# Kernel optimization log

Hardware: AMD Instinct MI355X
Metric: run time of the kernel (lower is better)

## Reference

```python
import jax, jax.numpy as jnp
import numpy as np

B, S, D_MODEL, D_HEAD = 8, 2048, 1024, 128
MAX_ROUNDS = 3
THRESH = 0.1
SCALE = 1.0 / np.sqrt(float(D_HEAD))


def setup_inputs() -> dict:
    key = jax.random.key(0)
    ks = jax.random.split(key, 12)

    def lin(k, out_d, in_d):
        # torch Linear weight layout [out, in], y = x @ W.T + b
        return (jax.random.normal(k, (out_d, in_d), jnp.float32) / np.sqrt(float(in_d))).astype(jnp.float32)

    thesis_w = lin(ks[3], D_HEAD, D_HEAD)
    return {
        "x": jax.random.normal(ks[0], (B, S, D_MODEL), jnp.float32),
        "wq": lin(ks[1], D_HEAD, D_MODEL),
        "wk": lin(ks[2], D_HEAD, D_MODEL),
        "wv": lin(ks[4], D_HEAD, D_MODEL),
        "thesis_w": thesis_w,  # antithesis weight is -thesis_w per __init__
        "thesis_b": 0.02 * jax.random.normal(ks[5], (D_HEAD,), jnp.float32),
        "anti_b": 0.02 * jax.random.normal(ks[6], (D_HEAD,), jnp.float32),
        "s_w1": lin(ks[7], D_HEAD, 3 * D_HEAD),
        "s_b1": jnp.zeros((D_HEAD,), jnp.float32),
        "s_w2": lin(ks[8], D_HEAD, D_HEAD),
        "s_b2": jnp.zeros((D_HEAD,), jnp.float32),
        "g_w": lin(ks[9], 1, 2 * D_HEAD),
        "g_b": jnp.zeros((1,), jnp.float32),
    }


def reference(x, wq, wk, wv, thesis_w, thesis_b, anti_b, s_w1, s_b1, s_w2, s_b2, g_w, g_b):
    # q/k/v projections (no bias)
    q = jnp.einsum("bsm,hm->bsh", x, wq)
    k = jnp.einsum("bsm,hm->bsh", x, wk)
    v = jnp.einsum("bsm,hm->bsh", x, wv)

    attn = jax.nn.softmax(jnp.einsum("bqh,bkh->bqk", q, k) * SCALE, axis=-1)
    # dropout is identity at eval time
    cur = jnp.einsum("bqk,bkh->bqh", attn, v)  # [B,S,Dh]

    # attn_weights and v never change across rounds, so thesis/antithesis are
    # round-invariant: compute the context projections once.
    context = cur
    thesis = context @ thesis_w.T + thesis_b
    anti = context @ (-thesis_w).T + anti_b  # antithesis weight = -thesis weight

    active = jnp.ones((B, S), dtype=bool)
    for _ in range(MAX_ROUNDS):
        # emulate `if not active_mask.any(): break` under jit
        any_active = jnp.any(active)
        am = active[..., None].astype(x.dtype)
        at, aa, ac = thesis * am, anti * am, cur * am

        h = jax.nn.relu(jnp.concatenate([at, aa, ac], axis=-1) @ s_w1.T + s_b1)
        synth = h @ s_w2.T + s_b2
        gate = jax.nn.sigmoid(jnp.concatenate([ac, synth], axis=-1) @ g_w.T + g_b)
        update = gate * (synth - ac) * 0.1
        new = cur + update  # applied to ALL tokens, matching original

        stable = jnp.linalg.norm(update, axis=-1) < THRESH  # new - cur == update
        cur = jnp.where(any_active, new, cur)
        active = jnp.where(any_active, active & ~stable, active)
    return cur
```

## Files before the change

### kernel.cpp

```cpp
#include <hip/hip_runtime.h>
#include <hip/hip_bf16.h>

#define B_   8
#define S_   2048
#define DM   1024
#define DH   128
#define BS_  16384
#define SCALE_  0.08838834764831845f
#define SCALE2_ 0.12751744f

typedef unsigned short u16;
typedef unsigned int   u32;
typedef _Float16 half8 __attribute__((ext_vector_type(8)));
typedef __bf16   bf16x8 __attribute__((ext_vector_type(8)));
typedef float    f32x4 __attribute__((ext_vector_type(4)));
typedef u32      u32x4 __attribute__((ext_vector_type(4)));

union H8 { u32x4 v; u32 u[4]; half8 h; bf16x8 b; };

__device__ __forceinline__ float bf2f(u16 u) {
    union { u32 i; float f; } w; w.i = ((u32)u) << 16; return w.f;
}
__device__ __forceinline__ void unpack8(uint4 v, float* f) {
    f[0] = bf2f(v.x & 0xffff); f[1] = bf2f(v.x >> 16);
    f[2] = bf2f(v.y & 0xffff); f[3] = bf2f(v.y >> 16);
    f[4] = bf2f(v.z & 0xffff); f[5] = bf2f(v.z >> 16);
    f[6] = bf2f(v.w & 0xffff); f[7] = bf2f(v.w >> 16);
}
__device__ __forceinline__ float ldE(const void* b, size_t i, int isbf16) {
    return isbf16 ? bf2f(((const u16*)b)[i]) : ((const float*)b)[i];
}
__device__ __forceinline__ void ld8(const void* b, size_t i, int isbf16, float* f) {
    if (isbf16) {
        unpack8(*(const uint4*)((const u16*)b + i), f);
    } else {
        float4 a = *(const float4*)((const float*)b + i);
        float4 c = *(const float4*)((const float*)b + i + 4);
        f[0] = a.x; f[1] = a.y; f[2] = a.z; f[3] = a.w;
        f[4] = c.x; f[5] = c.y; f[6] = c.z; f[7] = c.w;
    }
}
__device__ __forceinline__ u32 f2pk(float v) {
    _Float16 h = (_Float16)v;
    _Float16 l = (_Float16)(v - (float)h);
    union { _Float16 f; u16 u; } a, b; a.f = h; b.f = l;
    return ((u32)a.u << 16) | (u32)b.u;
}
__device__ __forceinline__ void split8(const float* f, u32x4& hi, u32x4& lo) {
    u32 H[8], L[8];
#pragma unroll
    for (int j = 0; j < 8; ++j) {
        _Float16 h = (_Float16)f[j];
        _Float16 l = (_Float16)(f[j] - (float)h);
        union { _Float16 x; u16 u; } a, b; a.x = h; b.x = l;
        H[j] = a.u; L[j] = b.u;
    }
    hi = (u32x4){H[0] | (H[1] << 16), H[2] | (H[3] << 16), H[4] | (H[5] << 16), H[6] | (H[7] << 16)};
    lo = (u32x4){L[0] | (L[1] << 16), L[2] | (L[3] << 16), L[4] | (L[5] << 16), L[6] | (L[7] << 16)};
}
__device__ __forceinline__ u32 permHI(u32 eB, u32 eA) { return __builtin_amdgcn_perm(eB, eA, 0x07060302u); }
__device__ __forceinline__ u16 f2h(float v) { union { _Float16 f; u16 u; } a; a.f = (_Float16)v; return a.u; }
__device__ __forceinline__ float h2f(u16 u) { union { _Float16 f; u16 u; } a; a.u = u; return (float)a.f; }

__global__ void init_kernel(const void* x, int* flag, int* active, int* counts) {
    int i = blockIdx.x * 256 + threadIdx.x;
    if (i < BS_) active[i] = 1;
    if (i < 4) counts[i] = (i == 0) ? BS_ : 0;
    if (i == 0) {
        const u16* w = (const u16*)x;
        int sane = 0;
        for (int t = 0; t < 256; ++t) {
            int e = (w[2 * t] >> 7) & 0xFF;
            if (e >= 100 && e <= 135) ++sane;
        }
        *flag = (sane >= 192) ? 1 : 0;
    }
}

__global__ __launch_bounds__(256) void prepack_w_kernel(
    const void* __restrict__ wq, const void* __restrict__ wk, const void* __restrict__ wv,
    const int* __restrict__ flag, u32x4* __restrict__ wpk)
{
    const int isb = *flag;
    const int gid = blockIdx.x * 256 + threadIdx.x;
    const int l  = gid & 63;
    const int t  = (gid >> 6) & 7;
    const int ks = (gid >> 9) & 31;
    const int z  = gid >> 14;
    const void* W = (z == 0) ? wq : (z == 1) ? wk : wv;
    const int row = 16 * t + (l & 15);
    const int k0  = ks * 32 + 8 * (l >> 4);
    const size_t base = ((((size_t)z * 32 + ks) * 16) + 2 * t) * 64 + l;
    if (isb) {
        uint4 v = *(const uint4*)((const u16*)W + (size_t)row * DM + k0);
        wpk[base] = (u32x4){v.x, v.y, v.z, v.w};
    } else {
        float f[8];
        ld8(W, (size_t)row * DM + k0, 0, f);
        u32x4 hi, lo;
        split8(f, hi, lo);
        wpk[base]      = hi;
        wpk[base + 64] = lo;
    }
}

__global__ __launch_bounds__(256) void qkv_kernel(
    const void* __restrict__ x, const u32x4* __restrict__ wpk,
    const int* __restrict__ flag, u32* __restrict__ qout,
    u32x4* __restrict__ kfrag, u32x4* __restrict__ vfrag)
{
    const int isb = *flag;
    const int z = blockIdx.z;
    const int bx = blockIdx.x;
    const int m0 = ((bx & 7) * 32 + (bx >> 3)) * 64;
    const int tid = threadIdx.x;
    const int wave = tid >> 6, lane = tid & 63;
    const int qd = lane >> 4, c = lane & 15;

    __shared__ u32x4 WL[2][8][2][64];
    __shared__ u16 TS[64][136];

    const u32x4* wz = wpk + (size_t)z * (32 * 16 * 64);
    const size_t arow = (size_t)(m0 + wave * 16 + c) * DM + 8 * qd;

#define STAGE_W(ks_, b_)                                                          \
    {                                                                             \
        const u32x4* _src = wz + ((size_t)(ks_) * 16 + 4 * wave) * 64 + lane;     \
        _Pragma("unroll")                                                         \
        for (int _j = 0; _j < 4; ++_j) {                                          \
            __builtin_amdgcn_global_load_lds(                                     \
                (const __attribute__((address_space(1))) u32*)(_src + _j * 64),   \
                (__attribute__((address_space(3))) u32*)&WL[b_][2 * wave + (_j >> 1)][_j & 1][0], \
                16, 0, 0);                                                        \
        }                                                                         \
    }
#define STAGE_WH(ks_, b_)                                                         \
    {                                                                             \
        _Pragma("unroll")                                                         \
        for (int _j = 0; _j < 2; ++_j) {                                          \
            __builtin_amdgcn_global_load_lds(                                     \
                (const __attribute__((address_space(1))) u32*)(                   \
                    wz + ((size_t)(ks_) * 16 + 2 * (2 * wave + _j)) * 64 + lane), \
                (__attribute__((address_space(3))) u32*)&WL[b_][2 * wave + _j][0][0], \
                16, 0, 0);                                                        \
        }                                                                         \
    }

    f32x4 acc[8] = {};

    if (isb) {
        const u16* xb = (const u16*)x;
        uint4 Ab = *(const uint4*)(xb + arow);
        STAGE_WH(0, 0);
        uint4 Abn = *(const uint4*)(xb + arow + 32);
        __syncthreads();
        for (int ks = 0; ks < 32; ++ks) {
            const int cb = ks & 1;
            if (ks + 1 < 32) STAGE_WH(ks + 1, cb ^ 1);
            H8 Ah; Ah.v = (u32x4){Ab.x, Ab.y, Ab.z, Ab.w};
#pragma unroll
            for (int t = 0; t < 8; ++t) {
                H8 bh; bh.v = WL[cb][t][0][lane];
                acc[t] = __builtin_amdgcn_mfma_f32_16x16x32_bf16(Ah.b, bh.b, acc[t], 0, 0, 0);
            }
            Ab = Abn;
            if (ks + 2 < 32) Abn = *(const uint4*)(xb + arow + (size_t)(ks + 2) * 32);
            __syncthreads();
        }
    } else {
        float Ar[8], Arn[8];
        ld8(x, arow, 0, Ar);
        STAGE_W(0, 0);
        ld8(x, arow + 32, 0, Arn);
        __syncthreads();
        for (int ks = 0; ks < 32; ++ks) {
            const int cb = ks & 1;
            if (ks + 1 < 32) STAGE_W(ks + 1, cb ^ 1);
            H8 Ah, Al;
            split8(Ar, Ah.v, Al.v);
#pragma unroll
            for (int t = 0; t < 8; ++t) {
                H8 bh, bl;
                bh.v = WL[cb][t][0][lane]; bl.v = WL[cb][t][1][lane];
                acc[t] = __builtin_amdgcn_mfma_f32_16x16x32_f16(Al.h, bh.h, acc[t], 0, 0, 0);
                acc[t] = __builtin_amdgcn_mfma_f32_16x16x32_f16(Ah.h, bl.h, acc[t], 0, 0, 0);
                acc[t] = __builtin_amdgcn_mfma_f32_16x16x32_f16(Ah.h, bh.h, acc[t], 0, 0, 0);
            }
#pragma unroll
            for (int j = 0; j < 8; ++j) Ar[j] = Arn[j];
            if (ks + 2 < 32) ld8(x, arow + (size_t)(ks + 2) * 32, 0, Arn);
            __syncthreads();
        }
    }
#undef STAGE_W
#undef STAGE_WH

    if (z == 0) {
#pragma unroll
        for (int r = 0; r < 4; ++r) {
            const int row = m0 + wave * 16 + qd * 4 + r;
            u32* op = qout + (size_t)row * DH + c;
#pragma unroll
            for (int t = 0; t < 8; ++t) op[t * 16] = f2pk(acc[t][r]);
        }
    } else {
#pragma unroll
        for (int t = 0; t < 8; ++t)
#pragma unroll
            for (int r = 0; r < 4; ++r)
                TS[wave * 16 + qd * 4 + r][16 * t + c] = f2h(acc[t][r]);
        __syncthreads();
        if (z == 1) {
#pragma unroll
            for (int i = 0; i < 4; ++i) {
                const int f = tid + 256 * i;
                const int lf = f & 63, ks = (f >> 6) & 3, sub = f >> 8;
                const int key = sub * 16 + (lf & 15);
                const int d0  = ks * 32 + 8 * (lf >> 4);
                u32 w[4];
#pragma unroll
                for (int q = 0; q < 4; ++q)
                    w[q] = (u32)TS[key][d0 + 2 * q] | ((u32)TS[key][d0 + 2 * q + 1] << 16);
                kfrag[((size_t)(m0 / 16 + sub) * 4 + ks) * 64 + lf] = (u32x4){w[0], w[1], w[2], w[3]};
            }
        } else {
#pragma unroll
            for (int i = 0; i < 4; ++i) {
                const int f = tid + 256 * i;
                const int lf = f & 63, t = (f >> 6) & 7, sub = f >> 9;
                const int kb2 = sub * 32 + 8 * (lf >> 4);
                const int dh  = 16 * t + (lf & 15);
                u32 w[4];
#pragma unroll
                for (int q = 0; q < 4; ++q)
                    w[q] = (u32)TS[kb2 + 2 * q][dh] | ((u32)TS[kb2 + 2 * q + 1][dh] << 16);
                vfrag[((size_t)(m0 / 32 + sub) * 8 + t) * 64 + lf] = (u32x4){w[0], w[1], w[2], w[3]};
            }
        }
    }
}

template <bool WRITE_PARTIAL>
__device__ __forceinline__ void attn_body(
    const u32* qp, const u32x4* __restrict__ kfrag, const u32x4* __restrict__ vfrag,
    u16* outO, u16* outL, float* cur,
    int b, int q0, int kt0, int kt1, int part)
{
    const int tid = threadIdx.x;
    const int wave = tid >> 6, lane = tid & 63;
    const int qd = lane >> 4, c = lane & 15;

    __shared__ u16 PB[4][531];

    H8 Qh[4];
    {
        const u32* qr = qp + ((size_t)b * S_ + q0 + wave * 16 + c) * DH;
#pragma unroll
        for (int ks = 0; ks < 4; ++ks) {
            uint4 e0 = *(const uint4*)(qr + ks * 32 + qd * 8);
            uint4 e1 = *(const uint4*)(qr + ks * 32 + qd * 8 + 4);
            Qh[ks].u[0] = permHI(e0.y, e0.x); Qh[ks].u[1] = permHI(e0.w, e0.z);
            Qh[ks].u[2] = permHI(e1.y, e1.x); Qh[ks].u[3] = permHI(e1.w, e1.z);
        }
    }

    f32x4 O[8] = {};
    float lsum[4] = {};

    const u32x4* kb0 = kfrag + (size_t)b * 128 * 256;
    const u32x4* vb0 = vfrag + (size_t)b * 64 * 512;

    for (int kt = kt0; kt < kt1; ++kt) {
        const u32x4* kf = kb0 + (size_t)kt * 512;
        const u32x4* vf = vb0 + (size_t)kt * 512;

        f32x4 S0 = {}, S1 = {};
#pragma unroll
        for (int ks = 0; ks < 4; ++ks) {
            H8 kh;
            kh.v = kf[ks * 64 + lane];
            S0 = __builtin_amdgcn_mfma_f32_16x16x32_f16(Qh[ks].h, kh.h, S0, 0, 0, 0);
            kh.v = kf[256 + ks * 64 + lane];
            S1 = __builtin_amdgcn_mfma_f32_16x16x32_f16(Qh[ks].h, kh.h, S1, 0, 0, 0);
        }

        u16* pw = PB[wave];
#pragma unroll
        for (int r = 0; r < 4; ++r) {
            float e0 = exp2f(fmaf(S0[r], SCALE2_, -4.0f));
            float e1 = exp2f(fmaf(S1[r], SCALE2_, -4.0f));
            lsum[r] += e0 + e1;
            pw[(4 * qd + r) * 33 + c]      = f2h(e0);
            pw[(4 * qd + r) * 33 + 16 + c] = f2h(e1);
        }

        u16 e[8];
#pragma unroll
        for (int j = 0; j < 8; ++j) e[j] = pw[c * 33 + 8 * qd + j];
        H8 Ph;
        Ph.u[0] = (u32)e[0] | ((u32)e[1] << 16);
        Ph.u[1] = (u32)e[2] | ((u32)e[3] << 16);
        Ph.u[2] = (u32)e[4] | ((u32)e[5] << 16);
        Ph.u[3] = (u32)e[6] | ((u32)e[7] << 16);

#pragma unroll
        for (int t = 0; t < 8; ++t) {
            H8 vh;
            vh.v = vf[t * 64 + lane];
            O[t] = __builtin_amdgcn_mfma_f32_16x16x32_f16(Ph.h, vh.h, O[t], 0, 0, 0);
        }
    }

    if (WRITE_PARTIAL) {
        float lred[4];
#pragma unroll
        for (int r = 0; r < 4; ++r) {
            float l = lsum[r];
            l += __shfl_xor(l, 1); l += __shfl_xor(l, 2);
            l += __shfl_xor(l, 4); l += __shfl_xor(l, 8);
            lred[r] = l;
        }
        const size_t rb = (size_t)b * S_ + q0 + wave * 16 + 4 * qd;
        u16* Op = outO + (size_t)part * ((size_t)BS_ * DH);
#pragma unroll
        for (int t = 0; t < 8; ++t)
#pragma unroll
            for (int r = 0; r < 4; ++r)
                Op[(rb + r) * DH + t * 16 + c] = f2h(O[t][r]);
        if (c == 0) {
            u16* lp = outL + (size_t)part * BS_;
#pragma unroll
            for (int r = 0; r < 4; ++r) lp[rb + r] = f2h(lred[r]);
        }
    } else {
        float linv[4];
#pragma unroll
        for (int r = 0; r < 4; ++r) {
            float l = lsum[r];
            l += __shfl_xor(l, 1); l += __shfl_xor(l, 2);
            l += __shfl_xor(l, 4); l += __shfl_xor(l, 8);
            linv[r] = 1.0f / l;
        }
        const size_t rb = (size_t)b * S_ + q0 + wave * 16 + 4 * qd;
#pragma unroll
        for (int t = 0; t < 8; ++t)
#pragma unroll
            for (int r = 0; r < 4; ++r)
                cur[(rb + r) * DH + t * 16 + c] = O[t][r] * linv[r];
    }
}

__global__ __launch_bounds__(256) void attn_kernel(
    const u32* qp, const u32x4* __restrict__ kfrag, const u32x4* __restrict__ vfrag, float* cur)
{
    const int rid = blockIdx.x + 32 * blockIdx.y;
    attn_body<false>(qp, kfrag, vfrag, nullptr, nullptr, cur,
                     rid & 7, ((rid >> 3) & 31) * 64, 0, S_ / 32, 0);
}

__global__ __launch_bounds__(256) void attn_split_kernel(
    const u32* qp, const u32x4* __restrict__ kfrag, const u32x4* __restrict__ vfrag,
    u16* __restrict__ Opart, u16* __restrict__ lpart)
{
    const int rid = blockIdx.x + 32 * (blockIdx.y + 8 * blockIdx.z);
    const int b    = rid & 7;
    const int qx   = (rid >> 3) & 31;
    const int part = rid >> 8;
    const int quart = S_ / 128;
    attn_body<true>(qp, kfrag, vfrag, Opart, lpart, nullptr,
                    b, qx * 64, part * quart, (part + 1) * quart, part);
}

__global__ __launch_bounds__(256) void combine_kernel(
    const u16* __restrict__ Opart, const u16* __restrict__ lpart,
    float* __restrict__ cur)
{
    const size_t N1 = (size_t)BS_ * DH;
    const size_t i0 = ((size_t)blockIdx.x * 256 + threadIdx.x) * 16;
    const int row = (int)(i0 >> 7);
    const float lt = h2f(lpart[row]) + h2f(lpart[BS_ + row])
                   + h2f(lpart[2 * BS_ + row]) + h2f(lpart[3 * BS_ + row]);
    const float linv = 1.0f / lt;
    float acc[16] = {};
#pragma unroll
    for (int p = 0; p < 4; ++p) {
        const u16* op = Opart + (size_t)p * N1 + i0;
        uint4 v0 = *(const uint4*)op;
        uint4 v1 = *(const uint4*)(op + 8);
        const u32 w[8] = {v0.x, v0.y, v0.z, v0.w, v1.x, v1.y, v1.z, v1.w};
#pragma unroll
        for (int j = 0; j < 8; ++j) {
            acc[2 * j]     += h2f((u16)(w[j] & 0xffff));
            acc[2 * j + 1] += h2f((u16)(w[j] >> 16));
        }
    }
#pragma unroll
    for (int t = 0; t < 4; ++t)
        *(float4*)(cur + i0 + t * 4) = make_float4(
            acc[4*t] * linv, acc[4*t+1] * linv, acc[4*t+2] * linv, acc[4*t+3] * linv);
}

__global__ __launch_bounds__(256) void prepack_rw_kernel(
    const void* __restrict__ tw, const void* __restrict__ w1, const void* __restrict__ w2,
    const int* __restrict__ flag, u32x4* __restrict__ pk)
{
    const int isb = *flag;
    const int gid = blockIdx.x * 256 + threadIdx.x;
    const int l = gid & 63, t = (gid >> 6) & 7, ks = (gid >> 9) & 3, mat = gid >> 11;
    const int row = 16 * t + (l & 15);
    const int k0  = ks * 32 + 8 * (l >> 4);
    float f[8];
    if (mat == 0)      ld8(tw, (size_t)row * DH + k0, isb, f);
    else if (mat <= 3) ld8(w1, (size_t)row * 384 + (mat - 1) * 128 + k0, isb, f);
    else               ld8(w2, (size_t)row * DH + k0, isb, f);
    u32x4 hi, lo;
    split8(f, hi, lo);
    const size_t base = (((size_t)mat * 4 + ks) * 16 + 2 * t) * 64 + l;
    pk[base] = hi; pk[base + 64] = lo;
}

struct Afrag { H8 h[4], l[4]; };
__device__ __forceinline__ void splitA(const float (&A)[4][8], Afrag& F) {
#pragma unroll
    for (int ks = 0; ks < 4; ++ks) split8(A[ks], F.h[ks].v, F.l[ks].v);
}
__device__ __forceinline__ void gemm_wb(const Afrag& F, const u32x4 (*WB)[16][64],
                                        const int lane, const int isb, f32x4 (&acc)[8])
{
#pragma unroll
    for (int ks = 0; ks < 4; ++ks) {
#pragma unroll
        for (int t = 0; t < 8; ++t) {
            H8 bh, bl;
            bh.v = WB[ks][2 * t][lane];
            bl.v = WB[ks][2 * t + 1][lane];
            acc[t] = __builtin_amdgcn_mfma_f32_16x16x32_f16(F.l[ks].h, bh.h, acc[t], 0, 0, 0);
            if (!isb)
                acc[t] = __builtin_amdgcn_mfma_f32_16x16x32_f16(F.h[ks].h, bl.h, acc[t], 0, 0, 0);
            acc[t] = __builtin_amdgcn_mfma_f32_16x16x32_f16(F.h[ks].h, bh.h, acc[t], 0, 0, 0);
        }
    }
}

__global__ __launch_bounds__(256) void round_kernel(
    const float* cur0, const float* curr,
    const u32x4* __restrict__ pk,
    const void* __restrict__ tb, const void* __restrict__ ab,
    const void* __restrict__ b1, const void* __restrict__ b2,
    const void* __restrict__ gw, const void* __restrict__ gb,
    const int* __restrict__ flag, int* active, int* counts, int r,
    float* cur_out, void* dout)
{
    const int isb = *flag;
    const int tok0 = blockIdx.x * 64;
    const int tid = threadIdx.x;
    const bool last = (dout != nullptr);

    if (counts[r] <= 0) {
        if (last) {
            for (int e = tid; e < 64 * DH; e += 256) {
                size_t idx = (size_t)tok0 * DH + e;
                float v = curr[idx];
                if (isb) ((__hip_bfloat16*)dout)[idx] = __float2bfloat16(v);
                else     ((float*)dout)[idx] = v;
            }
        }
        return;
    }

    const int wave = tid >> 6, lane = tid & 63;
    const int qd = lane >> 4, c = lane & 15;

    __shared__ u32x4 WB[4][16][64];
    __shared__ float T0S[64][132];
    __shared__ float HSS[64][132];
    __shared__ float actS[64], tbS[128], abS[128], b1S[128], b2S[128], gwS[256];
    __shared__ int blkcnt;

#define STAGE_RW(mat_)                                                             \
    {                                                                              \
        _Pragma("unroll")                                                          \
        for (int _j = 0; _j < 16; ++_j) {                                          \
            __builtin_amdgcn_global_load_lds(                                      \
                (const __attribute__((address_space(1))) u32*)(                    \
                    pk + (((size_t)(mat_) * 4 + wave) * 16 + _j) * 64 + lane),     \
                (__attribute__((address_space(3))) u32*)&WB[wave][_j][0],          \
                16, 0, 0);                                                         \
        }                                                                          \
    }

    STAGE_RW(0);
    if (tid < 64) actS[tid] = active[tok0 + tid] ? 1.0f : 0.0f;
    if (tid < 128) {
        tbS[tid] = ldE(tb, tid, isb); abS[tid] = ldE(ab, tid, isb);
        b1S[tid] = ldE(b1, tid, isb); b2S[tid] = ldE(b2, tid, isb);
    }
    gwS[tid] = ldE(gw, tid, isb);
    if (tid == 0) blkcnt = 0;
    const float gbf = ldE(gb, 0, isb);

    const int rowl = 16 * wave + c;
    const int hr   = 16 * wave + 4 * qd;

    float A1[4][8];
    {
        const float* cr = cur0 + (size_t)(tok0 + rowl) * DH;
#pragma unroll
        for (int ks = 0; ks < 4; ++ks) {
            *(float4*)&A1[ks][0] = *(const float4*)(cr + ks * 32 + 8 * qd);
            *(float4*)&A1[ks][4] = *(const float4*)(cr + ks * 32 + 8 * qd + 4);
        }
    }
    Afrag FA; splitA(A1, FA);
    __syncthreads();

    {
        f32x4 acc[8] = {};
        gemm_wb(FA, WB, lane, isb, acc);
#pragma unroll
        for (int t = 0; t < 8; ++t)
#pragma unroll
            for (int rr = 0; rr < 4; ++rr)
                T0S[hr + rr][16 * t + c] = acc[t][rr];
    }
    __syncthreads();
    STAGE_RW(1);

    f32x4 acc1[8] = {};
    const float am_r = actS[rowl];
    {
        float Ac[4][8];
#pragma unroll
        for (int ks = 0; ks < 4; ++ks)
#pragma unroll
            for (int j = 0; j < 8; ++j) {
                const int k = ks * 32 + 8 * qd + j;
                Ac[ks][j] = (T0S[rowl][k] + tbS[k]) * am_r;
            }
        Afrag FC; splitA(Ac, FC);
        __syncthreads();
        gemm_wb(FC, WB, lane, isb, acc1);
    }
    __syncthreads();
    STAGE_RW(2);
    {
        float Ac[4][8];
#pragma unroll
        for (int ks = 0; ks < 4; ++ks)
#pragma unroll
            for (int j = 0; j < 8; ++j) {
                const int k = ks * 32 + 8 * qd + j;
                Ac[ks][j] = (abS[k] - T0S[rowl][k]) * am_r;
            }
        Afrag FC; splitA(Ac, FC);
        __syncthreads();
        gemm_wb(FC, WB, lane, isb, acc1);
    }
    __syncthreads();
    STAGE_RW(3);
    {
        float Ac[4][8];
        const float* cr = curr + (size_t)(tok0 + rowl) * DH;
#pragma unroll
        for (int ks = 0; ks < 4; ++ks) {
            float4 a0 = *(const float4*)(cr + ks * 32 + 8 * qd);
            float4 a1 = *(const float4*)(cr + ks * 32 + 8 * qd + 4);
            Ac[ks][0] = a0.x * am_r; Ac[ks][1] = a0.y * am_r;
            Ac[ks][2] = a0.z * am_r; Ac[ks][3] = a0.w * am_r;
            Ac[ks][4] = a1.x * am_r; Ac[ks][5] = a1.y * am_r;
            Ac[ks][6] = a1.z * am_r; Ac[ks][7] = a1.w * am_r;
        }
        Afrag FC; splitA(Ac, FC);
        __syncthreads();
        gemm_wb(FC, WB, lane, isb, acc1);
    }
#pragma unroll
    for (int t = 0; t < 8; ++t)
#pragma unroll
        for (int rr = 0; rr < 4; ++rr)
            HSS[hr + rr][16 * t + c] = fmaxf(acc1[t][rr] + b1S[16 * t + c], 0.0f);
    __syncthreads();
    STAGE_RW(4);
    {
        float Ac[4][8];
#pragma unroll
        for (int ks = 0; ks < 4; ++ks) {
            const float* hp = &HSS[rowl][ks * 32 + 8 * qd];
            *(float4*)&Ac[ks][0] = *(const float4*)hp;
            *(float4*)&Ac[ks][4] = *(const float4*)(hp + 4);
        }
        Afrag FC; splitA(Ac, FC);
        __syncthreads();
        f32x4 acc2[8] = {};
        gemm_wb(FC, WB, lane, isb, acc2);
#pragma unroll
        for (int t = 0; t < 8; ++t)
#pragma unroll
            for (int rr = 0; rr < 4; ++rr)
                T0S[hr + rr][16 * t + c] = acc2[t][rr] + b2S[16 * t + c];
    }
    __syncthreads();

    const int tok = tid >> 2, d0 = (tid & 3) * 32;
    const float am = actS[tok];
    const float* cp = curr + (size_t)(tok0 + tok) * DH + d0;
    float cv[32];
#pragma unroll
    for (int t = 0; t < 8; ++t) {
        float4 vv = *(const float4*)(cp + t * 4);
        cv[t * 4] = vv.x; cv[t * 4 + 1] = vv.y; cv[t * 4 + 2] = vv.z; cv[t * 4 + 3] = vv.w;
    }
    const float* srow = &T0S[tok][d0];
    float gp = 0.0f;
#pragma unroll
    for (int e = 0; e < 32; ++e)
        gp += cv[e] * am * gwS[d0 + e] + srow[e] * gwS[128 + d0 + e];
    gp += __shfl_xor(gp, 1, 4);
    gp += __shfl_xor(gp, 2, 4);
    const float gate = 1.0f / (1.0f + __expf(-(gp + gbf)));
    float ss = 0.0f; float up[32];
#pragma unroll
    for (int e = 0; e < 32; ++e) {
        float u = gate * (srow[e] - cv[e] * am) * 0.1f;
        up[e] = u; ss += u * u;
    }
    ss += __shfl_xor(ss, 1, 4);
    ss += __shfl_xor(ss, 2, 4);
    const bool stable = sqrtf(ss) < 0.1f;

    if (last) {
        size_t off = (size_t)(tok0 + tok) * DH + d0;
        if (isb) {
            __hip_bfloat16* op = (__hip_bfloat16*)dout + off;
#pragma unroll
            for (int e = 0; e < 32; ++e) op[e] = __float2bfloat16(cv[e] + up[e]);
        } else {
            float* op = (float*)dout + off;
#pragma unroll
            for (int t = 0; t < 8; ++t)
                *(float4*)(op + t * 4) = make_float4(cv[t * 4] + up[t * 4], cv[t * 4 + 1] + up[t * 4 + 1],
                                                     cv[t * 4 + 2] + up[t * 4 + 2], cv[t * 4 + 3] + up[t * 4 + 3]);
        }
    } else {
        float* op = cur_out + (size_t)(tok0 + tok) * DH + d0;
#pragma unroll
        for (int t = 0; t < 8; ++t)
            *(float4*)(op + t * 4) = make_float4(cv[t * 4] + up[t * 4], cv[t * 4 + 1] + up[t * 4 + 1],
                                                 cv[t * 4 + 2] + up[t * 4 + 2], cv[t * 4 + 3] + up[t * 4 + 3]);
    }
    const int newact = (am > 0.0f && !stable) ? 1 : 0;
    if ((tid & 3) == 0) {
        active[tok0 + tok] = newact;
        if (newact) atomicAdd(&blkcnt, 1);
    }
    __syncthreads();
    if (tid == 0 && blkcnt > 0) atomicAdd(&counts[r + 1], blkcnt);
#undef STAGE_RW
}

extern "C" void kernel_launch(void* const* d_in, const int* in_sizes, int n_in,
                              void* d_out, int out_size, void* d_ws, size_t ws_size,
                              hipStream_t stream) {
    const void* x  = d_in[0];
    const void* wq = d_in[1];
    const void* wk = d_in[2];
    const void* wv = d_in[3];
    const void* tw = d_in[4];
    const void* tb = d_in[5];
    const void* ab = d_in[6];
    const void* w1 = d_in[7];
    const void* b1 = d_in[8];
    const void* w2 = d_in[9];
    const void* b2 = d_in[10];
    const void* gw = d_in[11];
    const void* gb = d_in[12];

    u32* ws = (u32*)d_ws;
    const size_t N1 = (size_t)BS_ * DH;
    u32* qp = ws;
    u32* kp = ws + N1;
    u32* vp = ws + 2 * N1;
    int* active = (int*)(ws + 3 * N1);
    int* counts = active + BS_;
    int* flag   = counts + 4;
    float* cur0  = (float*)qp;
    float* cur_r = (float*)kp;
    u16* Opart16 = (u16*)(ws + 3 * N1 + 32768);
    u16* lpart16 = (u16*)(ws + 5 * N1 + 32768);
    const bool big_ws = ws_size >= (size_t)42300000;
    u32x4* wpk = (u32x4*)(ws + 3 * N1 + 32768);
    u32x4* pkRW = (u32x4*)vp;
    u32x4* kfragP = (u32x4*)kp;
    u32x4* vfragP = (u32x4*)vp;

    init_kernel<<<dim3(BS_ / 256), 256, 0, stream>>>(x, flag, active, counts);
    prepack_w_kernel<<<dim3(192), 256, 0, stream>>>(wq, wk, wv, flag, wpk);
    qkv_kernel<<<dim3(BS_ / 64, 1, 3), 256, 0, stream>>>(x, wpk, flag, qp, kfragP, vfragP);
    if (big_ws) {
        attn_split_kernel<<<dim3(S_ / 64, B_, 4), 256, 0, stream>>>(qp, kfragP, vfragP, Opart16, lpart16);
        combine_kernel<<<dim3(512), 256, 0, stream>>>(Opart16, lpart16, cur0);
    } else {
        attn_kernel<<<dim3(S_ / 64, B_), 256, 0, stream>>>(qp, kfragP, vfragP, cur0);
    }
    prepack_rw_kernel<<<dim3(40), 256, 0, stream>>>(tw, w1, w2, flag, pkRW);
    round_kernel<<<dim3(BS_ / 64), 256, 0, stream>>>(
        cur0, cur0, pkRW, tb, ab, b1, b2, gw, gb, flag, active, counts, 0, cur_r, nullptr);
    round_kernel<<<dim3(BS_ / 64), 256, 0, stream>>>(
        cur0, cur_r, pkRW, tb, ab, b1, b2, gw, gb, flag, active, counts, 1, cur_r, nullptr);
    round_kernel<<<dim3(BS_ / 64), 256, 0, stream>>>(
        cur0, cur_r, pkRW, tb, ab, b1, b2, gw, gb, flag, active, counts, 2, cur_r, d_out);
}
```

Baseline: 266.5 us.

## Shrink LDS footprint in qkv and round kernels to raise occupancy

In qkv_kernel, the weight buffer and the transpose scratch now share one aliased LDS array, and the bf16 path stages two k-slices per barrier, halving the number of syncs. In round_kernel, the weight staging buffer is halved: the bf16 path loads only hi parts, and the fp32 path stages in two halves with extra barriers. The intermediate T0S/HSS tiles are stored as fp16 instead of fp32. The aim is to cut LDS use so more blocks fit per CU. The cost is extra barriers in the fp32 path and fp16 rounding of intermediates, which may change accuracy.

```diff
diff --git a/kernel.cpp b/kernel.cpp
--- a/kernel.cpp
+++ b/kernel.cpp
@@ -117,12 +117,26 @@
     const int wave = tid >> 6, lane = tid & 63;
     const int qd = lane >> 4, c = lane & 15;
 
-    __shared__ u32x4 WL[2][8][2][64];
-    __shared__ u16 TS[64][136];
+    __shared__ u32x4 WLraw[2][16][64];
+    u32x4 (*WLb)[2][8][64] = (u32x4(*)[2][8][64])WLraw;
+    u32x4 (*WLf)[8][2][64] = (u32x4(*)[8][2][64])WLraw;
+    u16 (*TS)[136] = (u16(*)[136])WLraw;
 
     const u32x4* wz = wpk + (size_t)z * (32 * 16 * 64);
     const size_t arow = (size_t)(m0 + wave * 16 + c) * DM + 8 * qd;
 
+#define STAGE2(i_, b_)                                                            \
+    {                                                                             \
+        _Pragma("unroll")                                                         \
+        for (int _j = 0; _j < 4; ++_j) {                                          \
+            const int _g = wave * 4 + _j, _ksub = _g >> 3, _t = _g & 7;           \
+            __builtin_amdgcn_global_load_lds(                                     \
+                (const __attribute__((address_space(1))) u32*)(                   \
+                    wz + ((size_t)(2 * (i_) + _ksub) * 16 + 2 * _t) * 64 + lane), \
+                (__attribute__((address_space(3))) u32*)&WLb[b_][_ksub][_t][0],   \
+                16, 0, 0);                                                        \
+        }                                                                         \
+    }
 #define STAGE_W(ks_, b_)                                                          \
     {                                                                             \
         const u32x4* _src = wz + ((size_t)(ks_) * 16 + 4 * wave) * 64 + lane;     \
@@ -130,41 +144,41 @@
         for (int _j = 0; _j < 4; ++_j) {                                          \
             __builtin_amdgcn_global_load_lds(                                     \
                 (const __attribute__((address_space(1))) u32*)(_src + _j * 64),   \
-                (__attribute__((address_space(3))) u32*)&WL[b_][2 * wave + (_j >> 1)][_j & 1][0], \
+                (__attribute__((address_space(3))) u32*)&WLf[b_][2 * wave + (_j >> 1)][_j & 1][0], \
                 16, 0, 0);                                                        \
         }                                                                         \
     }
-#define STAGE_WH(ks_, b_)                                                         \
-    {                                                                             \
-        _Pragma("unroll")                                                         \
-        for (int _j = 0; _j < 2; ++_j) {                                          \
-            __builtin_amdgcn_global_load_lds(                                     \
-                (const __attribute__((address_space(1))) u32*)(                   \
-                    wz + ((size_t)(ks_) * 16 + 2 * (2 * wave + _j)) * 64 + lane), \
-                (__attribute__((address_space(3))) u32*)&WL[b_][2 * wave + _j][0][0], \
-                16, 0, 0);                                                        \
-        }                                                                         \
-    }
 
     f32x4 acc[8] = {};
 
     if (isb) {
         const u16* xb = (const u16*)x;
-        uint4 Ab = *(const uint4*)(xb + arow);
-        STAGE_WH(0, 0);
-        uint4 Abn = *(const uint4*)(xb + arow + 32);
+        uint4 A0 = *(const uint4*)(xb + arow);
+        uint4 A1 = *(const uint4*)(xb + arow + 32);
+        STAGE2(0, 0);
+        uint4 A0n = *(const uint4*)(xb + arow + 64);
+        uint4 A1n = *(const uint4*)(xb + arow + 96);
         __syncthreads();
-        for (int ks = 0; ks < 32; ++ks) {
-            const int cb = ks & 1;
-            if (ks + 1 < 32) STAGE_WH(ks + 1, cb ^ 1);
-            H8 Ah; Ah.v = (u32x4){Ab.x, Ab.y, Ab.z, Ab.w};
+        for (int i = 0; i < 16; ++i) {
+            const int cb = i & 1;
+            if (i + 1 < 16) STAGE2(i + 1, cb ^ 1);
+            H8 Ah0; Ah0.v = (u32x4){A0.x, A0.y, A0.z, A0.w};
+            H8 Ah1; Ah1.v = (u32x4){A1.x, A1.y, A1.z, A1.w};
 #pragma unroll
             for (int t = 0; t < 8; ++t) {
-                H8 bh; bh.v = WL[cb][t][0][lane];
-                acc[t] = __builtin_amdgcn_mfma_f32_16x16x32_bf16(Ah.b, bh.b, acc[t], 0, 0, 0);
-            }
-            Ab = Abn;
-            if (ks + 2 < 32) Abn = *(const uint4*)(xb + arow + (size_t)(ks + 2) * 32);
+                H8 bh; bh.v = WLb[cb][0][t][lane];
+                acc[t] = __builtin_amdgcn_mfma_f32_16x16x32_bf16(Ah0.b, bh.b, acc[t], 0, 0, 0);
+            }
+#pragma unroll
+            for (int t = 0; t < 8; ++t) {
+                H8 bh; bh.v = WLb[cb][1][t][lane];
+                acc[t] = __builtin_amdgcn_mfma_f32_16x16x32_bf16(Ah1.b, bh.b, acc[t], 0, 0, 0);
+            }
+            A0 = A0n; A1 = A1n;
+            if (i + 2 < 16) {
+                A0n = *(const uint4*)(xb + arow + (size_t)(i + 2) * 64);
+                A1n = *(const uint4*)(xb + arow + (size_t)(i + 2) * 64 + 32);
+            }
             __syncthreads();
         }
     } else {
@@ -181,7 +195,7 @@
 #pragma unroll
             for (int t = 0; t < 8; ++t) {
                 H8 bh, bl;
-                bh.v = WL[cb][t][0][lane]; bl.v = WL[cb][t][1][lane];
+                bh.v = WLf[cb][t][0][lane]; bl.v = WLf[cb][t][1][lane];
                 acc[t] = __builtin_amdgcn_mfma_f32_16x16x32_f16(Al.h, bh.h, acc[t], 0, 0, 0);
                 acc[t] = __builtin_amdgcn_mfma_f32_16x16x32_f16(Ah.h, bl.h, acc[t], 0, 0, 0);
                 acc[t] = __builtin_amdgcn_mfma_f32_16x16x32_f16(Ah.h, bh.h, acc[t], 0, 0, 0);
@@ -192,8 +206,8 @@
             __syncthreads();
         }
     }
+#undef STAGE2
 #undef STAGE_W
-#undef STAGE_WH
 
     if (z == 0) {
 #pragma unroll
@@ -424,23 +438,6 @@
 #pragma unroll
     for (int ks = 0; ks < 4; ++ks) split8(A[ks], F.h[ks].v, F.l[ks].v);
 }
-__device__ __forceinline__ void gemm_wb(const Afrag& F, const u32x4 (*WB)[16][64],
-                                        const int lane, const int isb, f32x4 (&acc)[8])
-{
-#pragma unroll
-    for (int ks = 0; ks < 4; ++ks) {
-#pragma unroll
-        for (int t = 0; t < 8; ++t) {
-            H8 bh, bl;
-            bh.v = WB[ks][2 * t][lane];
-            bl.v = WB[ks][2 * t + 1][lane];
-            acc[t] = __builtin_amdgcn_mfma_f32_16x16x32_f16(F.l[ks].h, bh.h, acc[t], 0, 0, 0);
-            if (!isb)
-                acc[t] = __builtin_amdgcn_mfma_f32_16x16x32_f16(F.h[ks].h, bl.h, acc[t], 0, 0, 0);
-            acc[t] = __builtin_amdgcn_mfma_f32_16x16x32_f16(F.h[ks].h, bh.h, acc[t], 0, 0, 0);
-        }
-    }
-}
 
 __global__ __launch_bounds__(256) void round_kernel(
     const float* cur0, const float* curr,
@@ -471,25 +468,71 @@
     const int wave = tid >> 6, lane = tid & 63;
     const int qd = lane >> 4, c = lane & 15;
 
-    __shared__ u32x4 WB[4][16][64];
-    __shared__ float T0S[64][132];
-    __shared__ float HSS[64][132];
+    __shared__ u32x4 WB[4][8][64];
+    __shared__ u16 T0S[64][132];
+    __shared__ u16 HSS[64][132];
     __shared__ float actS[64], tbS[128], abS[128], b1S[128], b2S[128], gwS[256];
     __shared__ int blkcnt;
 
-#define STAGE_RW(mat_)                                                             \
-    {                                                                              \
-        _Pragma("unroll")                                                          \
-        for (int _j = 0; _j < 16; ++_j) {                                          \
-            __builtin_amdgcn_global_load_lds(                                      \
-                (const __attribute__((address_space(1))) u32*)(                    \
-                    pk + (((size_t)(mat_) * 4 + wave) * 16 + _j) * 64 + lane),     \
-                (__attribute__((address_space(3))) u32*)&WB[wave][_j][0],          \
-                16, 0, 0);                                                         \
-        }                                                                          \
-    }
-
-    STAGE_RW(0);
+    auto stageB = [&](int mat) {
+#pragma unroll
+        for (int j = 0; j < 8; ++j) {
+            __builtin_amdgcn_global_load_lds(
+                (const __attribute__((address_space(1))) u32*)(
+                    pk + (((size_t)mat * 4 + wave) * 16 + 2 * j) * 64 + lane),
+                (__attribute__((address_space(3))) u32*)&WB[wave][j][0],
+                16, 0, 0);
+        }
+    };
+    auto stageF = [&](int mat, int h) {
+#pragma unroll
+        for (int j = 0; j < 8; ++j) {
+            const int g = wave * 8 + j, kl = g >> 4, p = (g >> 3) & 1, t = g & 7;
+            __builtin_amdgcn_global_load_lds(
+                (const __attribute__((address_space(1))) u32*)(
+                    pk + (((size_t)mat * 4 + 2 * h + kl) * 16 + 2 * t + p) * 64 + lane),
+                (__attribute__((address_space(3))) u32*)&WB[kl * 2 + p][t][0],
+                16, 0, 0);
+        }
+    };
+    auto gemmB = [&](const Afrag& F, f32x4 (&acc)[8]) {
+#pragma unroll
+        for (int ks = 0; ks < 4; ++ks)
+#pragma unroll
+            for (int t = 0; t < 8; ++t) {
+                H8 bh; bh.v = WB[ks][t][lane];
+                acc[t] = __builtin_amdgcn_mfma_f32_16x16x32_f16(F.l[ks].h, bh.h, acc[t], 0, 0, 0);
+                acc[t] = __builtin_amdgcn_mfma_f32_16x16x32_f16(F.h[ks].h, bh.h, acc[t], 0, 0, 0);
+            }
+    };
+    auto gemmF = [&](const Afrag& F, int h, f32x4 (&acc)[8]) {
+#pragma unroll
+        for (int kl = 0; kl < 2; ++kl) {
+            const int ks = 2 * h + kl;
+#pragma unroll
+            for (int t = 0; t < 8; ++t) {
+                H8 bh, bl;
+                bh.v = WB[kl * 2][t][lane];
+                bl.v = WB[kl * 2 + 1][t][lane];
+                acc[t] = __builtin_amdgcn_mfma_f32_16x16x32_f16(F.l[ks].h, bh.h, acc[t], 0, 0, 0);
+                acc[t] = __builtin_amdgcn_mfma_f32_16x16x32_f16(F.h[ks].h, bl.h, acc[t], 0, 0, 0);
+                acc[t] = __builtin_amdgcn_mfma_f32_16x16x32_f16(F.h[ks].h, bh.h, acc[t], 0, 0, 0);
+            }
+        }
+    };
+    auto runGemm = [&](int mat, const Afrag& F, f32x4 (&acc)[8]) {
+        if (isb) {
+            gemmB(F, acc);
+        } else {
+            gemmF(F, 0, acc);
+            __syncthreads();
+            stageF(mat, 1);
+            __syncthreads();
+            gemmF(F, 1, acc);
+        }
+    };
+
+    if (isb) stageB(0); else stageF(0, 0);
     if (tid < 64) actS[tid] = active[tok0 + tid] ? 1.0f : 0.0f;
     if (tid < 128) {
         tbS[tid] = ldE(tb, tid, isb); abS[tid] = ldE(ab, tid, isb);
@@ -516,15 +559,15 @@
 
     {
         f32x4 acc[8] = {};
-        gemm_wb(FA, WB, lane, isb, acc);
+        runGemm(0, FA, acc);
 #pragma unroll
         for (int t = 0; t < 8; ++t)
 #pragma unroll
             for (int rr = 0; rr < 4; ++rr)
-                T0S[hr + rr][16 * t + c] = acc[t][rr];
+                T0S[hr + rr][16 * t + c] = f2h(acc[t][rr]);
     }
     __syncthreads();
-    STAGE_RW(1);
+    if (isb) stageB(1); else stageF(1, 0);
 
     f32x4 acc1[8] = {};
     const float am_r = actS[rowl];
@@ -535,14 +578,14 @@
 #pragma unroll
             for (int j = 0; j < 8; ++j) {
                 const int k = ks * 32 + 8 * qd + j;
-                Ac[ks][j] = (T0S[rowl][k] + tbS[k]) * am_r;
+                Ac[ks][j] = (h2f(T0S[rowl][k]) + tbS[k]) * am_r;
             }
         Afrag FC; splitA(Ac, FC);
         __syncthreads();
-        gemm_wb(FC, WB, lane, isb, acc1);
+        runGemm(1, FC, acc1);
     }
     __syncthreads();
-    STAGE_RW(2);
+    if (isb) stageB(2); else stageF(2, 0);
     {
         float Ac[4][8];
 #pragma unroll
@@ -550,14 +593,14 @@
 #pragma unroll
             for (int j = 0; j < 8; ++j) {
                 const int k = ks * 32 + 8 * qd + j;
-                Ac[ks][j] = (abS[k] - T0S[rowl][k]) * am_r;
+                Ac[ks][j] = (abS[k] - h2f(T0S[rowl][k])) * am_r;
             }
         Afrag FC; splitA(Ac, FC);
         __syncthreads();
-        gemm_wb(FC, WB, lane, isb, acc1);
+        runGemm(2, FC, acc1);
     }
     __syncthreads();
-    STAGE_RW(3);
+    if (isb) stageB(3); else stageF(3, 0);
     {
         float Ac[4][8];
         const float* cr = curr + (size_t)(tok0 + rowl) * DH;
@@ -572,32 +615,31 @@
         }
         Afrag FC; splitA(Ac, FC);
         __syncthreads();
-        gemm_wb(FC, WB, lane, isb, acc1);
+        runGemm(3, FC, acc1);
     }
 #pragma unroll
     for (int t = 0; t < 8; ++t)
 #pragma unroll
         for (int rr = 0; rr < 4; ++rr)
-            HSS[hr + rr][16 * t + c] = fmaxf(acc1[t][rr] + b1S[16 * t + c], 0.0f);
+            HSS[hr + rr][16 * t + c] = f2h(fmaxf(acc1[t][rr] + b1S[16 * t + c], 0.0f));
     __syncthreads();
-    STAGE_RW(4);
+    if (isb) stageB(4); else stageF(4, 0);
     {
         float Ac[4][8];
 #pragma unroll
-        for (int ks = 0; ks < 4; ++ks) {
-            const float* hp = &HSS[rowl][ks * 32 + 8 * qd];
-            *(float4*)&Ac[ks][0] = *(const float4*)hp;
-            *(float4*)&Ac[ks][4] = *(const float4*)(hp + 4);
-        }
+        for (int ks = 0; ks < 4; ++ks)
+#pragma unroll
+            for (int j = 0; j < 8; ++j)
+                Ac[ks][j] = h2f(HSS[rowl][ks * 32 + 8 * qd + j]);
         Afrag FC; splitA(Ac, FC);
         __syncthreads();
         f32x4 acc2[8] = {};
-        gemm_wb(FC, WB, lane, isb, acc2);
+        runGemm(4, FC, acc2);
 #pragma unroll
         for (int t = 0; t < 8; ++t)
 #pragma unroll
             for (int rr = 0; rr < 4; ++rr)
-                T0S[hr + rr][16 * t + c] = acc2[t][rr] + b2S[16 * t + c];
+                T0S[hr + rr][16 * t + c] = f2h(acc2[t][rr] + b2S[16 * t + c]);
     }
     __syncthreads();
 
@@ -610,7 +652,9 @@
         float4 vv = *(const float4*)(cp + t * 4);
         cv[t * 4] = vv.x; cv[t * 4 + 1] = vv.y; cv[t * 4 + 2] = vv.z; cv[t * 4 + 3] = vv.w;
     }
-    const float* srow = &T0S[tok][d0];
+    float srow[32];
+#pragma unroll
+    for (int e = 0; e < 32; ++e) srow[e] = h2f(T0S[tok][d0 + e]);
     float gp = 0.0f;
 #pragma unroll
     for (int e = 0; e < 32; ++e)
@@ -655,7 +699,6 @@
     }
     __syncthreads();
     if (tid == 0 && blkcnt > 0) atomicAdd(&counts[r + 1], blkcnt);
-#undef STAGE_RW
 }
 
 extern "C" void kernel_launch(void* const* d_in, const int* in_sizes, int n_in,
```

New measurement: 261.3 us. No clear change (-1.9%).
